# Performance work log

Hardware: AMD Instinct MI355X
Metric: run time of the kernel (lower is better)

Reference implementation:

```python
import jax, jax.numpy as jnp
import numpy as np

N_EMBD = 1024
N_HEAD = 16
T_LEN = 4096
BATCH = 1


def setup_inputs() -> dict:
    key = jax.random.key(0)
    ks = jax.random.split(key, 9)
    C = N_EMBD
    s = 1.0 / np.sqrt(C)
    inp = {
        "x": jax.random.normal(ks[0], (BATCH, T_LEN, C), dtype=jnp.float32),
        "wq": jax.random.normal(ks[1], (C, C), dtype=jnp.float32) * s,
        "bq": jax.random.normal(ks[2], (C,), dtype=jnp.float32) * s,
        "wk": jax.random.normal(ks[3], (C, C), dtype=jnp.float32) * s,
        "bk": jax.random.normal(ks[4], (C,), dtype=jnp.float32) * s,
        "wv": jax.random.normal(ks[5], (C, C), dtype=jnp.float32) * s,
        "bv": jax.random.normal(ks[6], (C,), dtype=jnp.float32) * s,
        "wp": jax.random.normal(ks[7], (C, C), dtype=jnp.float32) * s,
        "bp": jax.random.normal(ks[8], (C,), dtype=jnp.float32) * s,
    }
    return inp


def reference(x, wq, bq, wk, bk, wv, bv, wp, bp):
    B, T, C = x.shape
    H = N_HEAD
    D = C // H  # head_dim
    # torch nn.Linear: y = x @ W.T + b
    def lin(x, w, b):
        return jnp.einsum("btc,oc->bto", x, w) + b
    q = lin(x, wq, bq).reshape(B, T, H, D).transpose(0, 2, 1, 3)  # bhtd
    k = lin(x, wk, bk).reshape(B, T, H, D).transpose(0, 2, 1, 3)
    v = lin(x, wv, bv).reshape(B, T, H, D).transpose(0, 2, 1, 3)
    att = jnp.einsum("bhqd,bhkd->bhqk", q, k) / jnp.sqrt(jnp.float32(D))
    causal = jnp.tril(jnp.ones((T, T), dtype=bool))  # [T,T]
    att = jnp.where(causal[None, None, :, :], att, -jnp.inf)
    att = jax.nn.softmax(att, axis=-1)
    # dropout p=0.0 -> identity (eval equivalent)
    y = jnp.einsum("bhqk,bhkd->bhqd", att, v)
    y = y.transpose(0, 2, 1, 3).reshape(B, T, C)
    return jnp.einsum("btc,oc->bto", y, wp) + bp
```

## Files before the change

### kernel.cpp

```cpp
#include <hip/hip_runtime.h>
#include <stdint.h>

#define T_LEN 4096
#define C_DIM 1024
#define NH 16
#define CLOG2E 0.18033688011112042f

typedef uint16_t u16;
typedef __attribute__((ext_vector_type(4))) float f32x4;
typedef __attribute__((ext_vector_type(8))) __bf16 bf16x8;
typedef __attribute__((ext_vector_type(8))) uint16_t u16x8;
typedef __attribute__((ext_vector_type(4))) float fvec4;

static __device__ __forceinline__ u16 f2b(float f) {
  union { float f; uint32_t u; } v; v.f = f;
  uint32_t u = v.u;
  return (u16)((u + 0x7fffu + ((u >> 16) & 1u)) >> 16);
}

static __device__ __forceinline__ uint32_t cvtpk(float lo, float hi) {
  uint32_t r;
  asm("v_cvt_pk_bf16_f32 %0, %1, %2" : "=v"(r) : "v"(lo), "v"(hi));
  return r;
}

static __device__ __forceinline__ f32x4 mfma16(u16x8 a, u16x8 b, f32x4 c) {
  return __builtin_amdgcn_mfma_f32_16x16x32_bf16(
      __builtin_bit_cast(bf16x8, a), __builtin_bit_cast(bf16x8, b), c, 0, 0, 0);
}

static __device__ __forceinline__ void gload_lds16(const void* g, void* l) {
  __builtin_amdgcn_global_load_lds(
      (const __attribute__((address_space(1))) uint32_t*)g,
      (__attribute__((address_space(3))) uint32_t*)l, 16, 0, 0);
}

__global__ void cast_all(const float* __restrict__ x,
                         const float* __restrict__ wq, const float* __restrict__ wk,
                         const float* __restrict__ wv, const float* __restrict__ wp,
                         u16* __restrict__ xb,
                         u16* __restrict__ wqb, u16* __restrict__ wkb,
                         u16* __restrict__ wvb, u16* __restrict__ wpb) {
  int i = blockIdx.x * blockDim.x + threadIdx.x;
  if (i >= 131072) return;
  const int z = blockIdx.y;
  const float* in;
  u16* out;
  if (z < 4) {
    in  = (z == 0) ? wq  : (z == 1) ? wk  : (z == 2) ? wv  : wp;
    out = (z == 0) ? wqb : (z == 1) ? wkb : (z == 2) ? wvb : wpb;
  } else {
    in  = x  + (size_t)(z - 4) * 131072 * 8;
    out = xb + (size_t)(z - 4) * 131072 * 8;
  }
  const fvec4* p = (const fvec4*)(in + (size_t)i * 8);
  fvec4 a = p[0], b = p[1];
  u16x8 o;
  o[0] = f2b(a[0]); o[1] = f2b(a[1]); o[2] = f2b(a[2]); o[3] = f2b(a[3]);
  o[4] = f2b(b[0]); o[5] = f2b(b[1]); o[6] = f2b(b[2]); o[7] = f2b(b[3]);
  *(u16x8*)(out + (size_t)i * 8) = o;
}

__global__ __launch_bounds__(256) void gemm_qkv(
    const u16* __restrict__ xb,
    const u16* __restrict__ wqb, const u16* __restrict__ wkb, const u16* __restrict__ wvb,
    const float* __restrict__ bq, const float* __restrict__ bk, const float* __restrict__ bv,
    u16* __restrict__ qh, u16* __restrict__ kh, u16* __restrict__ vt)
{
  __shared__ u16 sA[128 * 32];
  __shared__ u16 sB[128 * 32];
  const int K = C_DIM;
  const int z = blockIdx.z;
  const u16* wb = (z == 0) ? wqb : (z == 1) ? wkb : wvb;
  const float* bias = (z == 0) ? bq : (z == 1) ? bk : bv;
  const int m0 = blockIdx.x * 128;
  const int n0 = blockIdx.y * 128;
  const int tid = threadIdx.x;
  const int lane = tid & 63;
  const int w = tid >> 6;
  const int wm = (w >> 1) * 64;
  const int wn = (w & 1) * 64;
  const int lr = lane & 15;
  const int lk = (lane >> 4) * 8;

  f32x4 acc[4][4];
#pragma unroll
  for (int m = 0; m < 4; ++m)
#pragma unroll
    for (int n = 0; n < 4; ++n) acc[m][n] = (f32x4){0.f, 0.f, 0.f, 0.f};

  const int srow = tid >> 2;
  const int scol = (tid & 3) * 8;
  const u16* gA = xb + (size_t)(m0 + srow) * K + scol;
  const u16* gB = wb + (size_t)(n0 + srow) * K + scol;

  for (int k0 = 0; k0 < K; k0 += 32) {
    gload_lds16(gA + k0,          &sA[tid * 8]);
    gload_lds16(gA + 64 * K + k0, &sA[2048 + tid * 8]);
    gload_lds16(gB + k0,          &sB[tid * 8]);
    gload_lds16(gB + 64 * K + k0, &sB[2048 + tid * 8]);
    __syncthreads();
    u16x8 af[4], bfr[4];
#pragma unroll
    for (int m = 0; m < 4; ++m) af[m]  = *(const u16x8*)&sA[(wm + m * 16 + lr) * 32 + lk];
#pragma unroll
    for (int n = 0; n < 4; ++n) bfr[n] = *(const u16x8*)&sB[(wn + n * 16 + lr) * 32 + lk];
#pragma unroll
    for (int m = 0; m < 4; ++m)
#pragma unroll
      for (int n = 0; n < 4; ++n) acc[m][n] = mfma16(af[m], bfr[n], acc[m][n]);
    __syncthreads();
  }

  const int lg = lane >> 4;
#pragma unroll
  for (int n = 0; n < 4; ++n) {
    const int o = n0 + wn + n * 16 + lr;
    const float bb = bias[o];
    const int h = o >> 6;
    const int d = o & 63;
#pragma unroll
    for (int m = 0; m < 4; ++m) {
      const int tb = m0 + wm + m * 16 + lg * 4;
      if (z == 2) {
        uint2 pk;
        pk.x = cvtpk(acc[m][n][0] + bb, acc[m][n][1] + bb);
        pk.y = cvtpk(acc[m][n][2] + bb, acc[m][n][3] + bb);
        *(uint2*)&vt[(size_t)o * T_LEN + tb] = pk;
      } else if (z == 0) {
#pragma unroll
        for (int r = 0; r < 4; ++r)
          qh[((size_t)h * T_LEN + tb + r) * 64 + d] = f2b((acc[m][n][r] + bb) * CLOG2E);
      } else {
#pragma unroll
        for (int r = 0; r < 4; ++r)
          kh[((size_t)h * T_LEN + tb + r) * 64 + d] = f2b(acc[m][n][r] + bb);
      }
    }
  }
}

__global__ __launch_bounds__(256) void gemm_proj(
    const u16* __restrict__ yb, const u16* __restrict__ wpb,
    const float* __restrict__ bp, float* __restrict__ out)
{
  __shared__ u16 sA[128 * 32];
  __shared__ u16 sB[64 * 32];
  const int K = C_DIM;
  const int m0 = blockIdx.x * 128;
  const int n0 = blockIdx.y * 64;
  const int tid = threadIdx.x;
  const int lane = tid & 63;
  const int w = tid >> 6;
  const int wm = w * 32;
  const int lr = lane & 15;
  const int lk = (lane >> 4) * 8;

  f32x4 acc[2][4];
#pragma unroll
  for (int m = 0; m < 2; ++m)
#pragma unroll
    for (int n = 0; n < 4; ++n) acc[m][n] = (f32x4){0.f, 0.f, 0.f, 0.f};

  const int srow = tid >> 2;
  const int scol = (tid & 3) * 8;
  const u16* gA = yb  + (size_t)(m0 + srow) * K + scol;
  const u16* gB = wpb + (size_t)(n0 + srow) * K + scol;

  for (int k0 = 0; k0 < K; k0 += 32) {
    gload_lds16(gA + k0,          &sA[tid * 8]);
    gload_lds16(gA + 64 * K + k0, &sA[2048 + tid * 8]);
    gload_lds16(gB + k0,          &sB[tid * 8]);
    __syncthreads();
    u16x8 af[2], bfr[4];
#pragma unroll
    for (int m = 0; m < 2; ++m) af[m]  = *(const u16x8*)&sA[(wm + m * 16 + lr) * 32 + lk];
#pragma unroll
    for (int n = 0; n < 4; ++n) bfr[n] = *(const u16x8*)&sB[(n * 16 + lr) * 32 + lk];
#pragma unroll
    for (int m = 0; m < 2; ++m)
#pragma unroll
      for (int n = 0; n < 4; ++n) acc[m][n] = mfma16(af[m], bfr[n], acc[m][n]);
    __syncthreads();
  }

  const int lg = lane >> 4;
#pragma unroll
  for (int n = 0; n < 4; ++n) {
    const int o = n0 + n * 16 + lr;
    const float bb = bp[o];
#pragma unroll
    for (int m = 0; m < 2; ++m) {
      const int tb = m0 + wm + m * 16 + lg * 4;
#pragma unroll
      for (int r = 0; r < 4; ++r)
        out[(size_t)(tb + r) * C_DIM + o] = acc[m][n][r] + bb;
    }
  }
}

__global__ __launch_bounds__(256) void attn_kernel(
    const u16* __restrict__ qh, const u16* __restrict__ kh, const u16* __restrict__ vt,
    u16* __restrict__ y)
{
  __shared__ char skb[2][8192];
  __shared__ char svb[2][8192];
  __shared__ u16 pp[4][16][64];
  const int bid = blockIdx.x;
  const int j = bid >> 3;
  const int h = ((bid & 7) << 1) + (j & 1);
  const int qb = 63 - (j >> 1);
  const int nt = qb + 1;
  const int tid = threadIdx.x;
  const int lane = tid & 63;
  const int w = tid >> 6;
  const int lr = lane & 15;
  const int lg = lane >> 4;
  const int sw = (lr & 7) << 4;
  const int qt0 = qb * 64 + w * 16;

  const int srow = tid >> 2;
  const int scb = (tid & 3) * 32;
  const int wo0 = srow * 128 + (scb ^ ((srow & 7) << 4));
  const int wo1 = srow * 128 + ((scb + 16) ^ ((srow & 7) << 4));
  const u16* gkbase = kh + ((size_t)h * T_LEN + srow) * 64 + (tid & 3) * 16;
  const u16* gvbase = vt + ((size_t)h * 64 + srow) * T_LEN + (tid & 3) * 16;
  char* ppb = (char*)&pp[w][0][0];

  const u16* qbase = qh + ((size_t)h * T_LEN + qt0 + lr) * 64 + lg * 8;
  u16x8 qf0 = *(const u16x8*)(qbase);
  u16x8 qf1 = *(const u16x8*)(qbase + 32);

  f32x4 oacc[4];
#pragma unroll
  for (int i = 0; i < 4; ++i) oacc[i] = (f32x4){0.f, 0.f, 0.f, 0.f};
  float mrow = -1e30f, lsum = 0.f;

  u16x8 ka = *(const u16x8*)(gkbase);
  u16x8 kb = *(const u16x8*)(gkbase + 8);
  u16x8 va = *(const u16x8*)(gvbase);
  u16x8 vb = *(const u16x8*)(gvbase + 8);
  *(u16x8*)(skb[0] + wo0) = ka; *(u16x8*)(skb[0] + wo1) = kb;
  *(u16x8*)(svb[0] + wo0) = va; *(u16x8*)(svb[0] + wo1) = vb;
  int cur = 0;

  for (int t = 0; t < nt; ++t) {
    __syncthreads();
    if (t + 1 < nt) {
      const size_t ko = (size_t)(t + 1) * 4096;
      ka = *(const u16x8*)(gkbase + ko);
      kb = *(const u16x8*)(gkbase + ko + 8);
      va = *(const u16x8*)(gvbase + (t + 1) * 64);
      vb = *(const u16x8*)(gvbase + (t + 1) * 64 + 8);
    }
    const char* skc = skb[cur];
    const char* svc = svb[cur];

    f32x4 sacc[4];
    __builtin_amdgcn_s_setprio(1);
#pragma unroll
    for (int i = 0; i < 4; ++i) {
      const int ro = (i * 16 + lr) * 128;
      u16x8 a0 = *(const u16x8*)(skc + ro + ((lg * 16) ^ sw));
      u16x8 a1 = *(const u16x8*)(skc + ro + ((lg * 16 + 64) ^ sw));
      f32x4 zz = (f32x4){0.f, 0.f, 0.f, 0.f};
      zz = mfma16(a0, qf0, zz);
      zz = mfma16(a1, qf1, zz);
      sacc[i] = zz;
    }
    __builtin_amdgcn_s_setprio(0);

    if (t == nt - 1) {
      const int qg = qt0 + lr;
      const int kt0 = t * 64;
#pragma unroll
      for (int i = 0; i < 4; ++i)
#pragma unroll
        for (int r = 0; r < 4; ++r) {
          const int kt = kt0 + i * 16 + lg * 4 + r;
          sacc[i][r] = (kt <= qg) ? sacc[i][r] : -1e30f;
        }
    }
    float x0 = fmaxf(fmaxf(sacc[0][0], sacc[0][1]), sacc[0][2]);
    float x1 = fmaxf(fmaxf(sacc[0][3], sacc[1][0]), sacc[1][1]);
    float x2 = fmaxf(fmaxf(sacc[1][2], sacc[1][3]), sacc[2][0]);
    float x3 = fmaxf(fmaxf(sacc[2][1], sacc[2][2]), sacc[2][3]);
    float x4 = fmaxf(fmaxf(sacc[3][0], sacc[3][1]), sacc[3][2]);
    float pm = fmaxf(fmaxf(fmaxf(x0, x1), fmaxf(x2, x3)), fmaxf(x4, sacc[3][3]));

    if (!__all(pm <= mrow)) {
      float pmf = fmaxf(pm, __shfl_xor(pm, 16));
      pmf = fmaxf(pmf, __shfl_xor(pmf, 32));
      const float mnew = fmaxf(mrow, pmf);
      const float sc = exp2f(mrow - mnew);
      lsum *= sc;
#pragma unroll
      for (int i = 0; i < 4; ++i) oacc[i] *= sc;
      mrow = mnew;
    }

    float t0 = 0.f, t1 = 0.f, t2 = 0.f, t3 = 0.f;
#pragma unroll
    for (int i = 0; i < 4; ++i) {
      float e0 = exp2f(sacc[i][0] - mrow);
      float e1 = exp2f(sacc[i][1] - mrow);
      float e2 = exp2f(sacc[i][2] - mrow);
      float e3 = exp2f(sacc[i][3] - mrow);
      t0 += e0; t1 += e1; t2 += e2; t3 += e3;
      uint2 pk;
      pk.x = cvtpk(e0, e1);
      pk.y = cvtpk(e2, e3);
      *(uint2*)(ppb + ((lr * 128 + i * 32 + lg * 8) ^ sw)) = pk;
    }
    lsum += (t0 + t1) + (t2 + t3);

    __builtin_amdgcn_s_setprio(1);
#pragma unroll
    for (int ks = 0; ks < 2; ++ks) {
      u16x8 pf = *(const u16x8*)(ppb + ((lr * 128 + lg * 16 + ks * 64) ^ sw));
#pragma unroll
      for (int dblk = 0; dblk < 4; ++dblk) {
        const int ro = (dblk * 16 + lr) * 128;
        u16x8 vf = *(const u16x8*)(svc + ro + ((lg * 16 + ks * 64) ^ sw));
        oacc[dblk] = mfma16(vf, pf, oacc[dblk]);
      }
    }
    __builtin_amdgcn_s_setprio(0);

    if (t + 1 < nt) {
      char* dk = skb[cur ^ 1];
      char* dv = svb[cur ^ 1];
      *(u16x8*)(dk + wo0) = ka; *(u16x8*)(dk + wo1) = kb;
      *(u16x8*)(dv + wo0) = va; *(u16x8*)(dv + wo1) = vb;
    }
    cur ^= 1;
  }

  lsum += __shfl_xor(lsum, 16);
  lsum += __shfl_xor(lsum, 32);
  const float inv = 1.0f / lsum;
#pragma unroll
  for (int dblk = 0; dblk < 4; ++dblk) {
    uint2 pk;
    pk.x = cvtpk(oacc[dblk][0] * inv, oacc[dblk][1] * inv);
    pk.y = cvtpk(oacc[dblk][2] * inv, oacc[dblk][3] * inv);
    *(uint2*)&y[(size_t)(qt0 + lr) * C_DIM + h * 64 + dblk * 16 + lg * 4] = pk;
  }
}

extern "C" void kernel_launch(void* const* d_in, const int* in_sizes, int n_in,
                              void* d_out, int out_size, void* d_ws, size_t ws_size,
                              hipStream_t stream) {
  const float* x  = (const float*)d_in[0];
  const float* wq = (const float*)d_in[1];
  const float* bq = (const float*)d_in[2];
  const float* wk = (const float*)d_in[3];
  const float* bk = (const float*)d_in[4];
  const float* wv = (const float*)d_in[5];
  const float* bv = (const float*)d_in[6];
  const float* wp = (const float*)d_in[7];
  const float* bp = (const float*)d_in[8];

  char* ws = (char*)d_ws;
  const size_t MB = 1024 * 1024;
  u16* xb  = (u16*)(ws + 0 * MB);
  u16* wqb = (u16*)(ws + 8 * MB);
  u16* wkb = (u16*)(ws + 10 * MB);
  u16* wvb = (u16*)(ws + 12 * MB);
  u16* wpb = (u16*)(ws + 14 * MB);
  u16* qh  = (u16*)(ws + 16 * MB);
  u16* kh  = (u16*)(ws + 24 * MB);
  u16* vt  = (u16*)(ws + 32 * MB);
  u16* y   = (u16*)(ws + 40 * MB);

  cast_all<<<dim3(512, 8), dim3(256), 0, stream>>>(
      x, wq, wk, wv, wp, xb, wqb, wkb, wvb, wpb);

  gemm_qkv<<<dim3(32, 8, 3), dim3(256), 0, stream>>>(
      xb, wqb, wkb, wvb, bq, bk, bv, qh, kh, vt);

  attn_kernel<<<dim3(1024), dim3(256), 0, stream>>>(qh, kh, vt, y);

  gemm_proj<<<dim3(32, 16), dim3(256), 0, stream>>>(y, wpb, bp, (float*)d_out);
}
```

Baseline: 147.1 us.

## Split long causal query blocks across two KV chunks with combine kernel

Query blocks in the upper half of the sequence are split into two work items: one covers KV tiles 0-31 and the other covers tiles 32 through the diagonal. Each writes unnormalized partial outputs plus row max and sum to workspace, and a new combine kernel merges them with log-sum-exp rescaling. Short blocks still run in one piece and write y directly. This caps per-block work at 32 tiles to cut the long-block tail and improve load balance across CUs. The cost is an extra launch, partial-output traffic through workspace that reuses buffers already consumed, and bf16 rounding of the partial outputs.

```diff
diff --git a/kernel.cpp b/kernel.cpp
--- a/kernel.cpp
+++ b/kernel.cpp
@@ -16,6 +16,11 @@
   union { float f; uint32_t u; } v; v.f = f;
   uint32_t u = v.u;
   return (u16)((u + 0x7fffu + ((u >> 16) & 1u)) >> 16);
+}
+
+static __device__ __forceinline__ float b2f(u16 b) {
+  union { uint32_t u; float f; } v; v.u = ((uint32_t)b) << 16;
+  return v.f;
 }
 
 static __device__ __forceinline__ uint32_t cvtpk(float lo, float hi) {
@@ -201,7 +206,7 @@
 
 __global__ __launch_bounds__(256) void attn_kernel(
     const u16* __restrict__ qh, const u16* __restrict__ kh, const u16* __restrict__ vt,
-    u16* __restrict__ y)
+    u16* __restrict__ y, u16* __restrict__ po, float* __restrict__ pml)
 {
   __shared__ char skb[2][8192];
   __shared__ char svb[2][8192];
@@ -209,8 +214,18 @@
   const int bid = blockIdx.x;
   const int j = bid >> 3;
   const int h = ((bid & 7) << 1) + (j & 1);
-  const int qb = 63 - (j >> 1);
-  const int nt = qb + 1;
+  const int i = j >> 1;
+  int qb, c0;
+  if (i < 32) { qb = 32 + i; c0 = 0; }
+  else {
+    const int k = (i - 32) >> 1;
+    if (((i - 32) & 1) == 0) { qb = 63 - k; c0 = 1; }
+    else                     { qb = 31 - k; c0 = -1; }
+  }
+  const int t0 = (c0 == 1) ? 32 : 0;
+  const int t1 = (c0 == 0) ? 32 : (qb + 1);
+  const bool hasdiag = (c0 != 0);
+
   const int tid = threadIdx.x;
   const int lane = tid & 63;
   const int w = tid >> 6;
@@ -233,20 +248,20 @@
 
   f32x4 oacc[4];
 #pragma unroll
-  for (int i = 0; i < 4; ++i) oacc[i] = (f32x4){0.f, 0.f, 0.f, 0.f};
+  for (int i2 = 0; i2 < 4; ++i2) oacc[i2] = (f32x4){0.f, 0.f, 0.f, 0.f};
   float mrow = -1e30f, lsum = 0.f;
 
-  u16x8 ka = *(const u16x8*)(gkbase);
-  u16x8 kb = *(const u16x8*)(gkbase + 8);
-  u16x8 va = *(const u16x8*)(gvbase);
-  u16x8 vb = *(const u16x8*)(gvbase + 8);
+  u16x8 ka = *(const u16x8*)(gkbase + (size_t)t0 * 4096);
+  u16x8 kb = *(const u16x8*)(gkbase + (size_t)t0 * 4096 + 8);
+  u16x8 va = *(const u16x8*)(gvbase + t0 * 64);
+  u16x8 vb = *(const u16x8*)(gvbase + t0 * 64 + 8);
   *(u16x8*)(skb[0] + wo0) = ka; *(u16x8*)(skb[0] + wo1) = kb;
   *(u16x8*)(svb[0] + wo0) = va; *(u16x8*)(svb[0] + wo1) = vb;
   int cur = 0;
 
-  for (int t = 0; t < nt; ++t) {
+  for (int t = t0; t < t1; ++t) {
     __syncthreads();
-    if (t + 1 < nt) {
+    if (t + 1 < t1) {
       const size_t ko = (size_t)(t + 1) * 4096;
       ka = *(const u16x8*)(gkbase + ko);
       kb = *(const u16x8*)(gkbase + ko + 8);
@@ -259,26 +274,26 @@
     f32x4 sacc[4];
     __builtin_amdgcn_s_setprio(1);
 #pragma unroll
-    for (int i = 0; i < 4; ++i) {
-      const int ro = (i * 16 + lr) * 128;
+    for (int i2 = 0; i2 < 4; ++i2) {
+      const int ro = (i2 * 16 + lr) * 128;
       u16x8 a0 = *(const u16x8*)(skc + ro + ((lg * 16) ^ sw));
       u16x8 a1 = *(const u16x8*)(skc + ro + ((lg * 16 + 64) ^ sw));
       f32x4 zz = (f32x4){0.f, 0.f, 0.f, 0.f};
       zz = mfma16(a0, qf0, zz);
       zz = mfma16(a1, qf1, zz);
-      sacc[i] = zz;
+      sacc[i2] = zz;
     }
     __builtin_amdgcn_s_setprio(0);
 
-    if (t == nt - 1) {
+    if (hasdiag && t == qb) {
       const int qg = qt0 + lr;
       const int kt0 = t * 64;
 #pragma unroll
-      for (int i = 0; i < 4; ++i)
+      for (int i2 = 0; i2 < 4; ++i2)
 #pragma unroll
         for (int r = 0; r < 4; ++r) {
-          const int kt = kt0 + i * 16 + lg * 4 + r;
-          sacc[i][r] = (kt <= qg) ? sacc[i][r] : -1e30f;
+          const int kt = kt0 + i2 * 16 + lg * 4 + r;
+          sacc[i2][r] = (kt <= qg) ? sacc[i2][r] : -1e30f;
         }
     }
     float x0 = fmaxf(fmaxf(sacc[0][0], sacc[0][1]), sacc[0][2]);
@@ -295,24 +310,24 @@
       const float sc = exp2f(mrow - mnew);
       lsum *= sc;
 #pragma unroll
-      for (int i = 0; i < 4; ++i) oacc[i] *= sc;
+      for (int i2 = 0; i2 < 4; ++i2) oacc[i2] *= sc;
       mrow = mnew;
     }
 
-    float t0 = 0.f, t1 = 0.f, t2 = 0.f, t3 = 0.f;
-#pragma unroll
-    for (int i = 0; i < 4; ++i) {
-      float e0 = exp2f(sacc[i][0] - mrow);
-      float e1 = exp2f(sacc[i][1] - mrow);
-      float e2 = exp2f(sacc[i][2] - mrow);
-      float e3 = exp2f(sacc[i][3] - mrow);
-      t0 += e0; t1 += e1; t2 += e2; t3 += e3;
+    float u0 = 0.f, u1 = 0.f, u2 = 0.f, u3 = 0.f;
+#pragma unroll
+    for (int i2 = 0; i2 < 4; ++i2) {
+      float e0 = exp2f(sacc[i2][0] - mrow);
+      float e1 = exp2f(sacc[i2][1] - mrow);
+      float e2 = exp2f(sacc[i2][2] - mrow);
+      float e3 = exp2f(sacc[i2][3] - mrow);
+      u0 += e0; u1 += e1; u2 += e2; u3 += e3;
       uint2 pk;
       pk.x = cvtpk(e0, e1);
       pk.y = cvtpk(e2, e3);
-      *(uint2*)(ppb + ((lr * 128 + i * 32 + lg * 8) ^ sw)) = pk;
-    }
-    lsum += (t0 + t1) + (t2 + t3);
+      *(uint2*)(ppb + ((lr * 128 + i2 * 32 + lg * 8) ^ sw)) = pk;
+    }
+    lsum += (u0 + u1) + (u2 + u3);
 
     __builtin_amdgcn_s_setprio(1);
 #pragma unroll
@@ -327,7 +342,7 @@
     }
     __builtin_amdgcn_s_setprio(0);
 
-    if (t + 1 < nt) {
+    if (t + 1 < t1) {
       char* dk = skb[cur ^ 1];
       char* dv = svb[cur ^ 1];
       *(u16x8*)(dk + wo0) = ka; *(u16x8*)(dk + wo1) = kb;
@@ -338,14 +353,77 @@
 
   lsum += __shfl_xor(lsum, 16);
   lsum += __shfl_xor(lsum, 32);
-  const float inv = 1.0f / lsum;
-#pragma unroll
-  for (int dblk = 0; dblk < 4; ++dblk) {
-    uint2 pk;
-    pk.x = cvtpk(oacc[dblk][0] * inv, oacc[dblk][1] * inv);
-    pk.y = cvtpk(oacc[dblk][2] * inv, oacc[dblk][3] * inv);
-    *(uint2*)&y[(size_t)(qt0 + lr) * C_DIM + h * 64 + dblk * 16 + lg * 4] = pk;
-  }
+
+  if (c0 < 0) {
+    const float inv = 1.0f / lsum;
+#pragma unroll
+    for (int dblk = 0; dblk < 4; ++dblk) {
+      uint2 pk;
+      pk.x = cvtpk(oacc[dblk][0] * inv, oacc[dblk][1] * inv);
+      pk.y = cvtpk(oacc[dblk][2] * inv, oacc[dblk][3] * inv);
+      *(uint2*)&y[(size_t)(qt0 + lr) * C_DIM + h * 64 + dblk * 16 + lg * 4] = pk;
+    }
+  } else {
+    const int slot = (((h << 5) + (qb - 32)) << 1) + c0;
+    u16* pob = po + (size_t)slot * 4096 + (size_t)(w * 16 + lr) * 64;
+#pragma unroll
+    for (int dblk = 0; dblk < 4; ++dblk) {
+      uint2 pk;
+      pk.x = cvtpk(oacc[dblk][0], oacc[dblk][1]);
+      pk.y = cvtpk(oacc[dblk][2], oacc[dblk][3]);
+      *(uint2*)(pob + dblk * 16 + lg * 4) = pk;
+    }
+    if (lg == 0) {
+      float2* pm2 = (float2*)pml;
+      pm2[slot * 64 + w * 16 + lr] = make_float2(mrow, lsum);
+    }
+  }
+}
+
+__global__ __launch_bounds__(256) void attn_combine(
+    const u16* __restrict__ po, const float* __restrict__ pml, u16* __restrict__ y)
+{
+  const int bid = blockIdx.x;
+  const int h = bid >> 5;
+  const int q5 = bid & 31;
+  const int tid = threadIdx.x;
+  const int row = tid >> 2;
+  const int dseg = (tid & 3) * 16;
+  const int slot0 = (((h << 5) + q5) << 1);
+  const float2 ml0 = ((const float2*)pml)[slot0 * 64 + row];
+  const float2 ml1 = ((const float2*)pml)[(slot0 + 1) * 64 + row];
+  const float m = fmaxf(ml0.x, ml1.x);
+  const float f0 = exp2f(ml0.x - m);
+  const float f1 = exp2f(ml1.x - m);
+  const float inv = 1.0f / (ml0.y * f0 + ml1.y * f1);
+  const float g0 = f0 * inv, g1 = f1 * inv;
+  const u16* p0 = po + (size_t)slot0 * 4096 + row * 64 + dseg;
+  const u16* p1 = p0 + 4096;
+  u16x8 a0 = *(const u16x8*)(p0);
+  u16x8 a1 = *(const u16x8*)(p0 + 8);
+  u16x8 b0 = *(const u16x8*)(p1);
+  u16x8 b1 = *(const u16x8*)(p1 + 8);
+  uint4 o0, o1;
+  float r0, r1;
+  r0 = b2f(a0[0]) * g0 + b2f(b0[0]) * g1; r1 = b2f(a0[1]) * g0 + b2f(b0[1]) * g1;
+  o0.x = cvtpk(r0, r1);
+  r0 = b2f(a0[2]) * g0 + b2f(b0[2]) * g1; r1 = b2f(a0[3]) * g0 + b2f(b0[3]) * g1;
+  o0.y = cvtpk(r0, r1);
+  r0 = b2f(a0[4]) * g0 + b2f(b0[4]) * g1; r1 = b2f(a0[5]) * g0 + b2f(b0[5]) * g1;
+  o0.z = cvtpk(r0, r1);
+  r0 = b2f(a0[6]) * g0 + b2f(b0[6]) * g1; r1 = b2f(a0[7]) * g0 + b2f(b0[7]) * g1;
+  o0.w = cvtpk(r0, r1);
+  r0 = b2f(a1[0]) * g0 + b2f(b1[0]) * g1; r1 = b2f(a1[1]) * g0 + b2f(b1[1]) * g1;
+  o1.x = cvtpk(r0, r1);
+  r0 = b2f(a1[2]) * g0 + b2f(b1[2]) * g1; r1 = b2f(a1[3]) * g0 + b2f(b1[3]) * g1;
+  o1.y = cvtpk(r0, r1);
+  r0 = b2f(a1[4]) * g0 + b2f(b1[4]) * g1; r1 = b2f(a1[5]) * g0 + b2f(b1[5]) * g1;
+  o1.z = cvtpk(r0, r1);
+  r0 = b2f(a1[6]) * g0 + b2f(b1[6]) * g1; r1 = b2f(a1[7]) * g0 + b2f(b1[7]) * g1;
+  o1.w = cvtpk(r0, r1);
+  u16* yp = y + (size_t)((q5 + 32) * 64 + row) * C_DIM + h * 64 + dseg;
+  *(uint4*)(yp) = o0;
+  *(uint4*)(yp + 8) = o1;
 }
 
 extern "C" void kernel_launch(void* const* d_in, const int* in_sizes, int n_in,
@@ -372,6 +450,8 @@
   u16* kh  = (u16*)(ws + 24 * MB);
   u16* vt  = (u16*)(ws + 32 * MB);
   u16* y   = (u16*)(ws + 40 * MB);
+  u16*   po  = (u16*)(ws + 0 * MB);
+  float* pml = (float*)(ws + 8 * MB);
 
   cast_all<<<dim3(512, 8), dim3(256), 0, stream>>>(
       x, wq, wk, wv, wp, xb, wqb, wkb, wvb, wpb);
@@ -379,7 +459,9 @@
   gemm_qkv<<<dim3(32, 8, 3), dim3(256), 0, stream>>>(
       xb, wqb, wkb, wvb, bq, bk, bv, qh, kh, vt);
 
-  attn_kernel<<<dim3(1024), dim3(256), 0, stream>>>(qh, kh, vt, y);
+  attn_kernel<<<dim3(1536), dim3(256), 0, stream>>>(qh, kh, vt, y, po, pml);
+
+  attn_combine<<<dim3(512), dim3(256), 0, stream>>>(po, pml, y);
 
   gemm_proj<<<dim3(32, 16), dim3(256), 0, stream>>>(y, wpb, bp, (float*)d_out);
 }
```

After: 144.1 us, median of 2. 2.0% less time.
